# Kernel optimization log

Hardware: AMD Instinct MI355X
Metric: run time of the kernel (lower is better)

Reference implementation:

```python
import jax, jax.numpy as jnp
import numpy as np

B, N, F, H, F_ = 4, 2048, 64, 4, 64


def setup_inputs() -> dict:
    key = jax.random.key(0)
    kx, ka, kw, ks, kn = jax.random.split(key, 5)
    X = jax.random.normal(kx, (B, N, F), dtype=jnp.float32)
    A = (jax.random.uniform(ka, (B, N, N)) < 0.05).astype(jnp.float32)
    A = jnp.maximum(A, jnp.eye(N, dtype=jnp.float32)[None])
    W = jax.random.normal(kw, (H, F, F_), dtype=jnp.float32) * 0.1
    a_self = jax.random.normal(ks, (H, F_), dtype=jnp.float32) * 0.1
    a_neigh = jax.random.normal(kn, (H, F_), dtype=jnp.float32) * 0.1
    return {"X": X, "A": A, "W": W, "a_self": a_self, "a_neigh": a_neigh}


def reference(X, A, W, a_self, a_neigh):
    # linear transform per head: [B,H,N,F_]
    lin = jnp.einsum('bnf,hfo->bhno', X, W)
    # additive attention scores
    s_self = jnp.einsum('bhno,ho->bhn', lin, a_self)[:, :, :, None]   # [B,H,N,1]
    s_neigh = jnp.einsum('bhno,ho->bhn', lin, a_neigh)[:, :, None, :]  # [B,H,1,N]
    dense = s_self + s_neigh                                           # [B,H,N,N]
    dense = jnp.where(dense >= 0, dense, 0.2 * dense)                  # LeakyReLU(0.2)
    BIG = jnp.float32(1e10)
    mask = jnp.exp(A * -BIG) * -BIG                                    # 0 where edge, -1e10 where no edge
    logits = dense + mask[:, None, :, :]
    attn = jax.nn.softmax(logits, axis=-1)
    # dropout is identity at inference (attn_dropout=0.0)
    feats = jnp.einsum('bhnm,bhmo->bhno', attn, lin)                   # [B,H,N,F_]
    feats = jax.nn.relu(feats)                                         # activation before concat
    b, h, n, f_ = feats.shape
    out = feats.transpose(0, 2, 1, 3).reshape(b, n, h * f_)            # concat heads
    return out
```

## Files before the change

kernel.cpp:

```cpp
#include <hip/hip_runtime.h>
#include <hip/hip_bf16.h>

#define BB 4
#define NN 2048
#define FF 64
#define HH 4
#define FO 64
#define CAP 256


__global__ __launch_bounds__(256) void BatchGraphAttention_84378927497895_kernel(
    const float* __restrict__ W, const float* __restrict__ a_self,
    const float* __restrict__ a_neigh, float* __restrict__ w_self,
    float* __restrict__ w_neigh) {
  int t = threadIdx.x;
  int h = t >> 6;
  const float* Wp = W + t * FO;
  const float* as = a_self + h * FO;
  const float* an = a_neigh + h * FO;
  float acc_s = 0.f, acc_n = 0.f;
#pragma unroll
  for (int o = 0; o < FO; ++o) {
    float w = Wp[o];
    acc_s += w * as[o];
    acc_n += w * an[o];
  }
  w_self[t] = acc_s;
  w_neigh[t] = acc_n;
}

__global__ __launch_bounds__(256) void BatchGraphAttention_84378927497895_kernel2(
    const float* __restrict__ X, const float* __restrict__ w_self,
    const float* __restrict__ w_neigh, float* __restrict__ s_self,
    float* __restrict__ s_neigh) {
  int bn = blockIdx.x;
  int t = threadIdx.x, h = t >> 6, f = t & 63;
  float x = X[(size_t)bn * FF + f];
  float vs = x * w_self[h * FF + f];
  float vn = x * w_neigh[h * FF + f];
#pragma unroll
  for (int off = 32; off > 0; off >>= 1) {
    vs += __shfl_down(vs, off, 64);
    vn += __shfl_down(vn, off, 64);
  }
  if (f == 0) {
    int b = bn >> 11, n = bn & (NN - 1);
    int bh = b * HH + h;
    s_self[bh * NN + n] = vs;
    s_neigh[bh * NN + n] = vn;
  }
}

__global__ __launch_bounds__(256) void BatchGraphAttention_84378927497895_kernel3(
    const float* __restrict__ A, const float* __restrict__ X,
    const float* __restrict__ s_self, const float* __restrict__ s_neigh,
    float* __restrict__ outScratch) {
  int bn = blockIdx.x;
  int b = bn >> 11;
  int n = bn & (NN - 1);
  __shared__ unsigned short idx[CAP];
  __shared__ float plt[CAP][4];
  __shared__ float red[4][HH][FF];
  __shared__ int cnt_s;
  int t = threadIdx.x;
  int lane = t & 63, wv = t >> 6;
  if (t == 0) cnt_s = 0;
  __syncthreads();

  {
    const float4* Ar4 = (const float4*)(A + (size_t)bn * NN);
#pragma unroll
    for (int it = 0; it < 2; ++it) {
      int q = t + it * 256;
      float4 v = Ar4[q];
      unsigned base = (unsigned)q * 4u;
      if (v.x != 0.f) { int p = atomicAdd(&cnt_s, 1); if (p < CAP) idx[p] = (unsigned short)(base + 0); }
      if (v.y != 0.f) { int p = atomicAdd(&cnt_s, 1); if (p < CAP) idx[p] = (unsigned short)(base + 1); }
      if (v.z != 0.f) { int p = atomicAdd(&cnt_s, 1); if (p < CAP) idx[p] = (unsigned short)(base + 2); }
      if (v.w != 0.f) { int p = atomicAdd(&cnt_s, 1); if (p < CAP) idx[p] = (unsigned short)(base + 3); }
    }
  }
  __syncthreads();
  int cnt = cnt_s;
  if (cnt > CAP) cnt = CAP;

  float inv;
  {
    int h = wv;
    int bh = b * HH + h;
    float ss = s_self[bh * NN + n];
    const float* snp = s_neigh + (size_t)bh * NN;

    float lmax = -1e30f;
    for (int j = lane; j < cnt; j += 64) {
      float lg = ss + snp[idx[j]];
      lg = (lg >= 0.f) ? lg : 0.2f * lg;
      plt[j][h] = lg;
      lmax = fmaxf(lmax, lg);
    }
#pragma unroll
    for (int off = 32; off > 0; off >>= 1)
      lmax = fmaxf(lmax, __shfl_xor(lmax, off, 64));

    float lsum = 0.f;
    for (int j = lane; j < cnt; j += 64) {
      float e = __expf(plt[j][h] - lmax);
      plt[j][h] = e;
      lsum += e;
    }
#pragma unroll
    for (int off = 32; off > 0; off >>= 1) lsum += __shfl_xor(lsum, off, 64);
    inv = 1.f / lsum;
  }
  __syncthreads();

  {
    const float* xp = X + (size_t)b * NN * FF + lane;
    float y0 = 0.f, y1 = 0.f, y2 = 0.f, y3 = 0.f;
    int j = wv;
    for (; j + 12 < cnt; j += 16) {
      int m0 = idx[j], m1 = idx[j + 4], m2 = idx[j + 8], m3 = idx[j + 12];
      float4 p0 = *(const float4*)plt[j];
      float4 p1 = *(const float4*)plt[j + 4];
      float4 p2 = *(const float4*)plt[j + 8];
      float4 p3 = *(const float4*)plt[j + 12];
      float x0 = xp[m0 * FF];
      float x1 = xp[m1 * FF];
      float x2 = xp[m2 * FF];
      float x3 = xp[m3 * FF];
      y0 += p0.x * x0; y1 += p0.y * x0; y2 += p0.z * x0; y3 += p0.w * x0;
      y0 += p1.x * x1; y1 += p1.y * x1; y2 += p1.z * x1; y3 += p1.w * x1;
      y0 += p2.x * x2; y1 += p2.y * x2; y2 += p2.z * x2; y3 += p2.w * x2;
      y0 += p3.x * x3; y1 += p3.y * x3; y2 += p3.z * x3; y3 += p3.w * x3;
    }
    for (; j < cnt; j += 4) {
      float4 p = *(const float4*)plt[j];
      float x = xp[idx[j] * FF];
      y0 += p.x * x; y1 += p.y * x; y2 += p.z * x; y3 += p.w * x;
    }
    red[wv][0][lane] = y0;
    red[wv][1][lane] = y1;
    red[wv][2][lane] = y2;
    red[wv][3][lane] = y3;
  }
  __syncthreads();

  {
    int h = wv, f = lane;
    float s = red[0][h][f] + red[1][h][f] + red[2][h][f] + red[3][h][f];
    outScratch[(size_t)bn * (HH * FO) + t] = s * inv;
  }
}

#define K4_ROWS 16
__global__ __launch_bounds__(256) void BatchGraphAttention_84378927497895_kernel4(
    const float* __restrict__ W, float* out) {
  int t = threadIdx.x;
  int h = t >> 6, o = t & 63;
  float w[FF];
  {
    const float* Wp = W + h * FF * FO + o;
#pragma unroll
    for (int f = 0; f < FF; ++f) w[f] = Wp[f * FO];
  }
  size_t base = (size_t)blockIdx.x * K4_ROWS;
  for (int r = 0; r < K4_ROWS; ++r) {
    const float4* yg = (const float4*)(out + (base + r) * (HH * FO) + h * FO);
    float acc = 0.f;
#pragma unroll
    for (int fq = 0; fq < FF / 4; ++fq) {
      float4 y4 = yg[fq];
      acc += w[4 * fq + 0] * y4.x;
      acc += w[4 * fq + 1] * y4.y;
      acc += w[4 * fq + 2] * y4.z;
      acc += w[4 * fq + 3] * y4.w;
    }
    acc = (acc > 0.f) ? acc : 0.f;
    out[(base + r) * (HH * FO) + t] = acc;
  }
}

extern "C" void kernel_launch(void* const* d_in, const int* in_sizes, int n_in,
                              void* d_out, int out_size, void* d_ws,
                              size_t ws_size, hipStream_t stream) {
  const float* X = (const float*)d_in[0];
  const float* A = (const float*)d_in[1];
  const float* W = (const float*)d_in[2];
  const float* a_self = (const float*)d_in[3];
  const float* a_neigh = (const float*)d_in[4];
  float* out = (float*)d_out;

  float* w_self = (float*)d_ws;
  float* w_neigh = w_self + HH * FF;
  float* s_self = w_neigh + HH * FF;
  float* s_neigh = s_self + (size_t)BB * HH * NN;

  BatchGraphAttention_84378927497895_kernel<<<1, 256, 0, stream>>>(
      W, a_self, a_neigh, w_self, w_neigh);
  BatchGraphAttention_84378927497895_kernel2<<<BB * NN, 256, 0, stream>>>(
      X, w_self, w_neigh, s_self, s_neigh);
  BatchGraphAttention_84378927497895_kernel3<<<BB * NN, 256, 0, stream>>>(
      A, X, s_self, s_neigh, out);
  BatchGraphAttention_84378927497895_kernel4<<<(BB * NN) / K4_ROWS, 256, 0, stream>>>(
      W, out);
}
```

Before: 153.0 us.

## Transpose attention scores to node-major layout and restructure sparse softmax aggregation

Stores the per-node attention scores as [B,N,H] so one float4 load fetches all four heads for a neighbour. Softmax now gives each thread one neighbour and all heads, reducing across waves through shared memory, instead of each wave looping over neighbours for one head. Other changes: the aggregation loop uses contiguous per-wave chunks with 8-way unrolled gathers, the adjacency row is read with nontemporal loads, and kernel2 handles 8 rows per block to cut launch count. This relies on cnt <= 256 = blockDim so that one pass per thread covers every neighbour, and it adds extra block-wide barriers.

```diff
diff --git a/kernel.cpp b/kernel.cpp
--- a/kernel.cpp
+++ b/kernel.cpp
@@ -7,6 +7,8 @@
 #define HH 4
 #define FO 64
 #define CAP 256
+
+typedef float f32x4 __attribute__((ext_vector_type(4)));
 
 
 __global__ __launch_bounds__(256) void BatchGraphAttention_84378927497895_kernel(
@@ -29,38 +31,43 @@
   w_neigh[t] = acc_n;
 }
 
+#define K1_ROWS 8
 __global__ __launch_bounds__(256) void BatchGraphAttention_84378927497895_kernel2(
     const float* __restrict__ X, const float* __restrict__ w_self,
-    const float* __restrict__ w_neigh, float* __restrict__ s_self,
-    float* __restrict__ s_neigh) {
-  int bn = blockIdx.x;
+    const float* __restrict__ w_neigh, float* __restrict__ s_selfT,
+    float* __restrict__ s_neighT) {
   int t = threadIdx.x, h = t >> 6, f = t & 63;
-  float x = X[(size_t)bn * FF + f];
-  float vs = x * w_self[h * FF + f];
-  float vn = x * w_neigh[h * FF + f];
-#pragma unroll
-  for (int off = 32; off > 0; off >>= 1) {
-    vs += __shfl_down(vs, off, 64);
-    vn += __shfl_down(vn, off, 64);
-  }
-  if (f == 0) {
-    int b = bn >> 11, n = bn & (NN - 1);
-    int bh = b * HH + h;
-    s_self[bh * NN + n] = vs;
-    s_neigh[bh * NN + n] = vn;
+  float wsv = w_self[h * FF + f];
+  float wnv = w_neigh[h * FF + f];
+  int base = blockIdx.x * K1_ROWS;
+  for (int r = 0; r < K1_ROWS; ++r) {
+    int bn = base + r;
+    float x = X[(size_t)bn * FF + f];
+    float vs = x * wsv;
+    float vn = x * wnv;
+#pragma unroll
+    for (int off = 32; off > 0; off >>= 1) {
+      vs += __shfl_down(vs, off, 64);
+      vn += __shfl_down(vn, off, 64);
+    }
+    if (f == 0) {
+      s_selfT[bn * HH + h] = vs;
+      s_neighT[bn * HH + h] = vn;
+    }
   }
 }
 
 __global__ __launch_bounds__(256) void BatchGraphAttention_84378927497895_kernel3(
     const float* __restrict__ A, const float* __restrict__ X,
-    const float* __restrict__ s_self, const float* __restrict__ s_neigh,
+    const float* __restrict__ s_selfT, const float* __restrict__ s_neighT,
     float* __restrict__ outScratch) {
   int bn = blockIdx.x;
   int b = bn >> 11;
-  int n = bn & (NN - 1);
   __shared__ unsigned short idx[CAP];
-  __shared__ float plt[CAP][4];
+  __shared__ float4 plt4[CAP];
   __shared__ float red[4][HH][FF];
+  __shared__ float4 mred4[4];
+  __shared__ float4 sred4[4];
   __shared__ int cnt_s;
   int t = threadIdx.x;
   int lane = t & 63, wv = t >> 6;
@@ -68,11 +75,11 @@
   __syncthreads();
 
   {
-    const float4* Ar4 = (const float4*)(A + (size_t)bn * NN);
+    const f32x4* Ar4 = (const f32x4*)(A + (size_t)bn * NN);
 #pragma unroll
     for (int it = 0; it < 2; ++it) {
       int q = t + it * 256;
-      float4 v = Ar4[q];
+      f32x4 v = __builtin_nontemporal_load(Ar4 + q);
       unsigned base = (unsigned)q * 4u;
       if (v.x != 0.f) { int p = atomicAdd(&cnt_s, 1); if (p < CAP) idx[p] = (unsigned short)(base + 0); }
       if (v.y != 0.f) { int p = atomicAdd(&cnt_s, 1); if (p < CAP) idx[p] = (unsigned short)(base + 1); }
@@ -83,58 +90,95 @@
   __syncthreads();
   int cnt = cnt_s;
   if (cnt > CAP) cnt = CAP;
-
-  float inv;
-  {
-    int h = wv;
-    int bh = b * HH + h;
-    float ss = s_self[bh * NN + n];
-    const float* snp = s_neigh + (size_t)bh * NN;
-
-    float lmax = -1e30f;
-    for (int j = lane; j < cnt; j += 64) {
-      float lg = ss + snp[idx[j]];
-      lg = (lg >= 0.f) ? lg : 0.2f * lg;
-      plt[j][h] = lg;
-      lmax = fmaxf(lmax, lg);
-    }
-#pragma unroll
-    for (int off = 32; off > 0; off >>= 1)
-      lmax = fmaxf(lmax, __shfl_xor(lmax, off, 64));
-
-    float lsum = 0.f;
-    for (int j = lane; j < cnt; j += 64) {
-      float e = __expf(plt[j][h] - lmax);
-      plt[j][h] = e;
-      lsum += e;
-    }
-#pragma unroll
-    for (int off = 32; off > 0; off >>= 1) lsum += __shfl_xor(lsum, off, 64);
-    inv = 1.f / lsum;
-  }
-  __syncthreads();
-
-  {
+  bool act = t < cnt;
+
+  float4 ss4 = ((const float4*)s_selfT)[bn];
+  const float4* snT = (const float4*)s_neighT + (size_t)b * NN;
+
+  float l0 = -1e30f, l1 = -1e30f, l2 = -1e30f, l3 = -1e30f;
+  if (act) {
+    float4 sn = snT[idx[t]];
+    l0 = ss4.x + sn.x; l0 = (l0 >= 0.f) ? l0 : 0.2f * l0;
+    l1 = ss4.y + sn.y; l1 = (l1 >= 0.f) ? l1 : 0.2f * l1;
+    l2 = ss4.z + sn.z; l2 = (l2 >= 0.f) ? l2 : 0.2f * l2;
+    l3 = ss4.w + sn.w; l3 = (l3 >= 0.f) ? l3 : 0.2f * l3;
+  }
+  float m0 = l0, m1 = l1, m2 = l2, m3 = l3;
+#pragma unroll
+  for (int off = 32; off > 0; off >>= 1) {
+    m0 = fmaxf(m0, __shfl_xor(m0, off, 64));
+    m1 = fmaxf(m1, __shfl_xor(m1, off, 64));
+    m2 = fmaxf(m2, __shfl_xor(m2, off, 64));
+    m3 = fmaxf(m3, __shfl_xor(m3, off, 64));
+  }
+  if (lane == 0) mred4[wv] = make_float4(m0, m1, m2, m3);
+  __syncthreads();
+  {
+    float4 a0 = mred4[0], a1 = mred4[1], a2 = mred4[2], a3 = mred4[3];
+    m0 = fmaxf(fmaxf(a0.x, a1.x), fmaxf(a2.x, a3.x));
+    m1 = fmaxf(fmaxf(a0.y, a1.y), fmaxf(a2.y, a3.y));
+    m2 = fmaxf(fmaxf(a0.z, a1.z), fmaxf(a2.z, a3.z));
+    m3 = fmaxf(fmaxf(a0.w, a1.w), fmaxf(a2.w, a3.w));
+  }
+  float e0 = 0.f, e1 = 0.f, e2 = 0.f, e3 = 0.f;
+  if (act) {
+    e0 = __expf(l0 - m0);
+    e1 = __expf(l1 - m1);
+    e2 = __expf(l2 - m2);
+    e3 = __expf(l3 - m3);
+    plt4[t] = make_float4(e0, e1, e2, e3);
+  }
+  float s0 = e0, s1 = e1, s2 = e2, s3 = e3;
+#pragma unroll
+  for (int off = 32; off > 0; off >>= 1) {
+    s0 += __shfl_xor(s0, off, 64);
+    s1 += __shfl_xor(s1, off, 64);
+    s2 += __shfl_xor(s2, off, 64);
+    s3 += __shfl_xor(s3, off, 64);
+  }
+  if (lane == 0) sred4[wv] = make_float4(s0, s1, s2, s3);
+  __syncthreads();
+  float4 inv4;
+  {
+    float4 a0 = sred4[0], a1 = sred4[1], a2 = sred4[2], a3 = sred4[3];
+    inv4.x = 1.f / (a0.x + a1.x + a2.x + a3.x);
+    inv4.y = 1.f / (a0.y + a1.y + a2.y + a3.y);
+    inv4.z = 1.f / (a0.z + a1.z + a2.z + a3.z);
+    inv4.w = 1.f / (a0.w + a1.w + a2.w + a3.w);
+  }
+
+  {
+    int chunk = ((cnt + 31) >> 5) << 3;
+    int jb = wv * chunk;
+    int je = jb + chunk;
+    if (je > cnt) je = cnt;
     const float* xp = X + (size_t)b * NN * FF + lane;
     float y0 = 0.f, y1 = 0.f, y2 = 0.f, y3 = 0.f;
-    int j = wv;
-    for (; j + 12 < cnt; j += 16) {
-      int m0 = idx[j], m1 = idx[j + 4], m2 = idx[j + 8], m3 = idx[j + 12];
-      float4 p0 = *(const float4*)plt[j];
-      float4 p1 = *(const float4*)plt[j + 4];
-      float4 p2 = *(const float4*)plt[j + 8];
-      float4 p3 = *(const float4*)plt[j + 12];
-      float x0 = xp[m0 * FF];
-      float x1 = xp[m1 * FF];
-      float x2 = xp[m2 * FF];
-      float x3 = xp[m3 * FF];
+    int j = jb;
+    for (; j + 7 < je; j += 8) {
+      ushort4 ma = *(const ushort4*)(idx + j);
+      ushort4 mb = *(const ushort4*)(idx + j + 4);
+      float4 p0 = plt4[j],     p1 = plt4[j + 1], p2 = plt4[j + 2], p3 = plt4[j + 3];
+      float4 p4 = plt4[j + 4], p5 = plt4[j + 5], p6 = plt4[j + 6], p7 = plt4[j + 7];
+      float x0 = xp[ma.x * FF];
+      float x1 = xp[ma.y * FF];
+      float x2 = xp[ma.z * FF];
+      float x3 = xp[ma.w * FF];
+      float x4 = xp[mb.x * FF];
+      float x5 = xp[mb.y * FF];
+      float x6 = xp[mb.z * FF];
+      float x7 = xp[mb.w * FF];
       y0 += p0.x * x0; y1 += p0.y * x0; y2 += p0.z * x0; y3 += p0.w * x0;
       y0 += p1.x * x1; y1 += p1.y * x1; y2 += p1.z * x1; y3 += p1.w * x1;
       y0 += p2.x * x2; y1 += p2.y * x2; y2 += p2.z * x2; y3 += p2.w * x2;
       y0 += p3.x * x3; y1 += p3.y * x3; y2 += p3.z * x3; y3 += p3.w * x3;
-    }
-    for (; j < cnt; j += 4) {
-      float4 p = *(const float4*)plt[j];
+      y0 += p4.x * x4; y1 += p4.y * x4; y2 += p4.z * x4; y3 += p4.w * x4;
+      y0 += p5.x * x5; y1 += p5.y * x5; y2 += p5.z * x5; y3 += p5.w * x5;
+      y0 += p6.x * x6; y1 += p6.y * x6; y2 += p6.z * x6; y3 += p6.w * x6;
+      y0 += p7.x * x7; y1 += p7.y * x7; y2 += p7.z * x7; y3 += p7.w * x7;
+    }
+    for (; j < je; ++j) {
+      float4 p = plt4[j];
       float x = xp[idx[j] * FF];
       y0 += p.x * x; y1 += p.y * x; y2 += p.z * x; y3 += p.w * x;
     }
@@ -148,7 +192,9 @@
   {
     int h = wv, f = lane;
     float s = red[0][h][f] + red[1][h][f] + red[2][h][f] + red[3][h][f];
-    outScratch[(size_t)bn * (HH * FO) + t] = s * inv;
+    float invh = (wv == 0) ? inv4.x : (wv == 1) ? inv4.y : (wv == 2) ? inv4.z
+                                                                     : inv4.w;
+    outScratch[(size_t)bn * (HH * FO) + t] = s * invh;
   }
 }
 
@@ -192,15 +238,15 @@
 
   float* w_self = (float*)d_ws;
   float* w_neigh = w_self + HH * FF;
-  float* s_self = w_neigh + HH * FF;
-  float* s_neigh = s_self + (size_t)BB * HH * NN;
+  float* s_selfT = w_neigh + HH * FF;
+  float* s_neighT = s_selfT + (size_t)BB * NN * HH;
 
   BatchGraphAttention_84378927497895_kernel<<<1, 256, 0, stream>>>(
       W, a_self, a_neigh, w_self, w_neigh);
-  BatchGraphAttention_84378927497895_kernel2<<<BB * NN, 256, 0, stream>>>(
-      X, w_self, w_neigh, s_self, s_neigh);
+  BatchGraphAttention_84378927497895_kernel2<<<(BB * NN) / K1_ROWS, 256, 0, stream>>>(
+      X, w_self, w_neigh, s_selfT, s_neighT);
   BatchGraphAttention_84378927497895_kernel3<<<BB * NN, 256, 0, stream>>>(
-      A, X, s_self, s_neigh, out);
+      A, X, s_selfT, s_neighT, out);
   BatchGraphAttention_84378927497895_kernel4<<<(BB * NN) / K4_ROWS, 256, 0, stream>>>(
       W, out);
 }
```

Measured after the change: 167.4 us. 1.09x slower.

## Assign one wavefront per attention row and transpose score layout

Applied to the files above, without the earlier changes.

The attention kernel now gives each wavefront its own row, not one row per block. It compacts the adjacency with ballot/mbcnt instead of shared-memory atomics, keeps the softmax weights in registers, and broadcasts them with readlane during aggregation, which removes all block barriers. The score arrays are stored node-major with all four heads interleaved, so one float4 gather fetches every head's neighbour score. The score kernel handles 8 rows per block, and adjacency loads are nontemporal. The catch is that each wave walks its neighbours serially with scalar broadcasts, so X gathers from different waves no longer share work the way they did when four waves split one row.

```diff
diff --git a/kernel.cpp b/kernel.cpp
--- a/kernel.cpp
+++ b/kernel.cpp
@@ -7,6 +7,8 @@
 #define HH 4
 #define FO 64
 #define CAP 256
+
+typedef float f32x4 __attribute__((ext_vector_type(4)));
 
 
 __global__ __launch_bounds__(256) void BatchGraphAttention_84378927497895_kernel(
@@ -29,127 +31,148 @@
   w_neigh[t] = acc_n;
 }
 
+#define K1_ROWS 8
 __global__ __launch_bounds__(256) void BatchGraphAttention_84378927497895_kernel2(
     const float* __restrict__ X, const float* __restrict__ w_self,
-    const float* __restrict__ w_neigh, float* __restrict__ s_self,
-    float* __restrict__ s_neigh) {
-  int bn = blockIdx.x;
+    const float* __restrict__ w_neigh, float* __restrict__ s_selfT,
+    float* __restrict__ s_neighT) {
   int t = threadIdx.x, h = t >> 6, f = t & 63;
-  float x = X[(size_t)bn * FF + f];
-  float vs = x * w_self[h * FF + f];
-  float vn = x * w_neigh[h * FF + f];
-#pragma unroll
-  for (int off = 32; off > 0; off >>= 1) {
-    vs += __shfl_down(vs, off, 64);
-    vn += __shfl_down(vn, off, 64);
-  }
-  if (f == 0) {
-    int b = bn >> 11, n = bn & (NN - 1);
-    int bh = b * HH + h;
-    s_self[bh * NN + n] = vs;
-    s_neigh[bh * NN + n] = vn;
-  }
-}
-
-__global__ __launch_bounds__(256) void BatchGraphAttention_84378927497895_kernel3(
+  float wsv = w_self[h * FF + f];
+  float wnv = w_neigh[h * FF + f];
+  int base = blockIdx.x * K1_ROWS;
+  for (int r = 0; r < K1_ROWS; ++r) {
+    int bn = base + r;
+    float x = X[(size_t)bn * FF + f];
+    float vs = x * wsv;
+    float vn = x * wnv;
+#pragma unroll
+    for (int off = 32; off > 0; off >>= 1) {
+      vs += __shfl_down(vs, off, 64);
+      vn += __shfl_down(vn, off, 64);
+    }
+    if (f == 0) {
+      s_selfT[bn * HH + h] = vs;
+      s_neighT[bn * HH + h] = vn;
+    }
+  }
+}
+
+__global__ __launch_bounds__(256, 6) void BatchGraphAttention_84378927497895_kernel3(
     const float* __restrict__ A, const float* __restrict__ X,
-    const float* __restrict__ s_self, const float* __restrict__ s_neigh,
+    const float* __restrict__ s_selfT, const float* __restrict__ s_neighT,
     float* __restrict__ outScratch) {
-  int bn = blockIdx.x;
-  int b = bn >> 11;
-  int n = bn & (NN - 1);
-  __shared__ unsigned short idx[CAP];
-  __shared__ float plt[CAP][4];
-  __shared__ float red[4][HH][FF];
-  __shared__ int cnt_s;
+  __shared__ unsigned short idxAll[4][CAP];
   int t = threadIdx.x;
   int lane = t & 63, wv = t >> 6;
-  if (t == 0) cnt_s = 0;
-  __syncthreads();
-
+  int bn = blockIdx.x * 4 + wv;
+  int b = bn >> 11;
+  unsigned short* idxw = idxAll[wv];
+
+  int cnt = 0;
   {
-    const float4* Ar4 = (const float4*)(A + (size_t)bn * NN);
-#pragma unroll
-    for (int it = 0; it < 2; ++it) {
-      int q = t + it * 256;
-      float4 v = Ar4[q];
-      unsigned base = (unsigned)q * 4u;
-      if (v.x != 0.f) { int p = atomicAdd(&cnt_s, 1); if (p < CAP) idx[p] = (unsigned short)(base + 0); }
-      if (v.y != 0.f) { int p = atomicAdd(&cnt_s, 1); if (p < CAP) idx[p] = (unsigned short)(base + 1); }
-      if (v.z != 0.f) { int p = atomicAdd(&cnt_s, 1); if (p < CAP) idx[p] = (unsigned short)(base + 2); }
-      if (v.w != 0.f) { int p = atomicAdd(&cnt_s, 1); if (p < CAP) idx[p] = (unsigned short)(base + 3); }
-    }
-  }
-  __syncthreads();
-  int cnt = cnt_s;
-  if (cnt > CAP) cnt = CAP;
-
-  float inv;
-  {
-    int h = wv;
-    int bh = b * HH + h;
-    float ss = s_self[bh * NN + n];
-    const float* snp = s_neigh + (size_t)bh * NN;
-
-    float lmax = -1e30f;
-    for (int j = lane; j < cnt; j += 64) {
-      float lg = ss + snp[idx[j]];
-      lg = (lg >= 0.f) ? lg : 0.2f * lg;
-      plt[j][h] = lg;
-      lmax = fmaxf(lmax, lg);
-    }
+    const f32x4* Ar4 = (const f32x4*)(A + (size_t)bn * NN);
+#pragma unroll
+    for (int i = 0; i < 8; ++i) {
+      f32x4 v = __builtin_nontemporal_load(Ar4 + i * 64 + lane);
+      int mbase = i * 256 + lane * 4;
+#pragma unroll
+      for (int c = 0; c < 4; ++c) {
+        float vc = (c == 0) ? v.x : (c == 1) ? v.y : (c == 2) ? v.z : v.w;
+        bool p = (vc != 0.f);
+        unsigned long long mk = __ballot(p);
+        int rk = __builtin_amdgcn_mbcnt_hi(
+            (unsigned)(mk >> 32),
+            __builtin_amdgcn_mbcnt_lo((unsigned)mk, 0u));
+        int pos = cnt + rk;
+        if (p && pos < CAP) idxw[pos] = (unsigned short)(mbase + c);
+        cnt += (int)__popcll(mk);
+      }
+    }
+    if (cnt > CAP) cnt = CAP;
+  }
+
+  float4 ss4 = ((const float4*)s_selfT)[bn];
+  const float4* snT = (const float4*)s_neighT + (size_t)b * NN;
+  int mreg[4];
+  float ev[4][HH];
+#pragma unroll
+  for (int r = 0; r < 4; ++r) {
+    int j = (r << 6) + lane;
+    int m = idxw[j];
+    bool val = j < cnt;
+    if (!val) m = 0;
+    mreg[r] = m;
+    float4 sn = snT[m];
+    float a0 = ss4.x + sn.x; a0 = (a0 >= 0.f) ? a0 : 0.2f * a0;
+    float a1 = ss4.y + sn.y; a1 = (a1 >= 0.f) ? a1 : 0.2f * a1;
+    float a2 = ss4.z + sn.z; a2 = (a2 >= 0.f) ? a2 : 0.2f * a2;
+    float a3 = ss4.w + sn.w; a3 = (a3 >= 0.f) ? a3 : 0.2f * a3;
+    ev[r][0] = val ? a0 : -1e30f;
+    ev[r][1] = val ? a1 : -1e30f;
+    ev[r][2] = val ? a2 : -1e30f;
+    ev[r][3] = val ? a3 : -1e30f;
+  }
+  float mh[HH], sh[HH];
+#pragma unroll
+  for (int h = 0; h < HH; ++h) {
+    float mm = fmaxf(fmaxf(ev[0][h], ev[1][h]), fmaxf(ev[2][h], ev[3][h]));
 #pragma unroll
     for (int off = 32; off > 0; off >>= 1)
-      lmax = fmaxf(lmax, __shfl_xor(lmax, off, 64));
-
-    float lsum = 0.f;
-    for (int j = lane; j < cnt; j += 64) {
-      float e = __expf(plt[j][h] - lmax);
-      plt[j][h] = e;
-      lsum += e;
-    }
-#pragma unroll
-    for (int off = 32; off > 0; off >>= 1) lsum += __shfl_xor(lsum, off, 64);
-    inv = 1.f / lsum;
-  }
-  __syncthreads();
-
-  {
-    const float* xp = X + (size_t)b * NN * FF + lane;
-    float y0 = 0.f, y1 = 0.f, y2 = 0.f, y3 = 0.f;
-    int j = wv;
-    for (; j + 12 < cnt; j += 16) {
-      int m0 = idx[j], m1 = idx[j + 4], m2 = idx[j + 8], m3 = idx[j + 12];
-      float4 p0 = *(const float4*)plt[j];
-      float4 p1 = *(const float4*)plt[j + 4];
-      float4 p2 = *(const float4*)plt[j + 8];
-      float4 p3 = *(const float4*)plt[j + 12];
-      float x0 = xp[m0 * FF];
-      float x1 = xp[m1 * FF];
-      float x2 = xp[m2 * FF];
-      float x3 = xp[m3 * FF];
-      y0 += p0.x * x0; y1 += p0.y * x0; y2 += p0.z * x0; y3 += p0.w * x0;
-      y0 += p1.x * x1; y1 += p1.y * x1; y2 += p1.z * x1; y3 += p1.w * x1;
-      y0 += p2.x * x2; y1 += p2.y * x2; y2 += p2.z * x2; y3 += p2.w * x2;
-      y0 += p3.x * x3; y1 += p3.y * x3; y2 += p3.z * x3; y3 += p3.w * x3;
-    }
-    for (; j < cnt; j += 4) {
-      float4 p = *(const float4*)plt[j];
-      float x = xp[idx[j] * FF];
-      y0 += p.x * x; y1 += p.y * x; y2 += p.z * x; y3 += p.w * x;
-    }
-    red[wv][0][lane] = y0;
-    red[wv][1][lane] = y1;
-    red[wv][2][lane] = y2;
-    red[wv][3][lane] = y3;
-  }
-  __syncthreads();
-
-  {
-    int h = wv, f = lane;
-    float s = red[0][h][f] + red[1][h][f] + red[2][h][f] + red[3][h][f];
-    outScratch[(size_t)bn * (HH * FO) + t] = s * inv;
-  }
+      mm = fmaxf(mm, __shfl_xor(mm, off, 64));
+    mh[h] = mm;
+  }
+#pragma unroll
+  for (int r = 0; r < 4; ++r)
+#pragma unroll
+    for (int h = 0; h < HH; ++h) ev[r][h] = __expf(ev[r][h] - mh[h]);
+#pragma unroll
+  for (int h = 0; h < HH; ++h) {
+    float s = (ev[0][h] + ev[1][h]) + (ev[2][h] + ev[3][h]);
+#pragma unroll
+    for (int off = 32; off > 0; off >>= 1) s += __shfl_xor(s, off, 64);
+    sh[h] = 1.f / s;
+  }
+#pragma unroll
+  for (int r = 0; r < 4; ++r)
+#pragma unroll
+    for (int h = 0; h < HH; ++h) ev[r][h] *= sh[h];
+
+  float y0 = 0.f, y1 = 0.f, y2 = 0.f, y3 = 0.f;
+  const float* xp = X + (size_t)b * NN * FF + lane;
+#define PVROUND(R)                                                            \
+  {                                                                           \
+    int lim = cnt - (R << 6);                                                 \
+    if (lim > 0) {                                                            \
+      if (lim > 64) lim = 64;                                                 \
+      _Pragma("unroll 4") for (int jl = 0; jl < lim; ++jl) {                  \
+        int mm = __builtin_amdgcn_readlane(mreg[R], jl);                      \
+        float p0 = __uint_as_float(                                           \
+            __builtin_amdgcn_readlane(__float_as_uint(ev[R][0]), jl));        \
+        float p1 = __uint_as_float(                                           \
+            __builtin_amdgcn_readlane(__float_as_uint(ev[R][1]), jl));        \
+        float p2 = __uint_as_float(                                           \
+            __builtin_amdgcn_readlane(__float_as_uint(ev[R][2]), jl));        \
+        float p3 = __uint_as_float(                                           \
+            __builtin_amdgcn_readlane(__float_as_uint(ev[R][3]), jl));        \
+        float x = xp[mm * FF];                                                \
+        y0 += p0 * x;                                                         \
+        y1 += p1 * x;                                                         \
+        y2 += p2 * x;                                                         \
+        y3 += p3 * x;                                                         \
+      }                                                                       \
+    }                                                                         \
+  }
+  PVROUND(0)
+  PVROUND(1)
+  PVROUND(2)
+  PVROUND(3)
+#undef PVROUND
+
+  size_t ob = (size_t)bn * (HH * FO);
+  outScratch[ob + 0 * 64 + lane] = y0;
+  outScratch[ob + 1 * 64 + lane] = y1;
+  outScratch[ob + 2 * 64 + lane] = y2;
+  outScratch[ob + 3 * 64 + lane] = y3;
 }
 
 #define K4_ROWS 16
@@ -192,15 +215,15 @@
 
   float* w_self = (float*)d_ws;
   float* w_neigh = w_self + HH * FF;
-  float* s_self = w_neigh + HH * FF;
-  float* s_neigh = s_self + (size_t)BB * HH * NN;
+  float* s_selfT = w_neigh + HH * FF;
+  float* s_neighT = s_selfT + (size_t)BB * NN * HH;
 
   BatchGraphAttention_84378927497895_kernel<<<1, 256, 0, stream>>>(
       W, a_self, a_neigh, w_self, w_neigh);
-  BatchGraphAttention_84378927497895_kernel2<<<BB * NN, 256, 0, stream>>>(
-      X, w_self, w_neigh, s_self, s_neigh);
-  BatchGraphAttention_84378927497895_kernel3<<<BB * NN, 256, 0, stream>>>(
-      A, X, s_self, s_neigh, out);
+  BatchGraphAttention_84378927497895_kernel2<<<(BB * NN) / K1_ROWS, 256, 0, stream>>>(
+      X, w_self, w_neigh, s_selfT, s_neighT);
+  BatchGraphAttention_84378927497895_kernel3<<<(BB * NN) / 4, 256, 0, stream>>>(
+      A, X, s_selfT, s_neighT, out);
   BatchGraphAttention_84378927497895_kernel4<<<(BB * NN) / K4_ROWS, 256, 0, stream>>>(
       W, out);
 }
```

New measurement: 178.0 us. +16.3%, slower.
